# Performance work log

Measured on AMD Instinct MI355X. Metric: run time of the kernel, lower is better.

## Reference

```python
import jax, jax.numpy as jnp
import numpy as np
import math

S, W, H = 256, 128, 768   # sentence, word, hidden (hidden fixed to 768 by PositionalEncoding)
TOPK = 3                  # len(inputs) > 2 branch: fuse 3 nearest sentences


def positional_encoding(length, d_model):
    # Standard sinusoidal PE, identical to the torch buffer construction.
    pos = jnp.arange(length, dtype=jnp.float32)[:, None]                      # [L,1]
    div = jnp.exp(jnp.arange(0, d_model, 2, dtype=jnp.float32)
                  * (-math.log(10000.0) / d_model))                           # [H/2]
    pe = jnp.zeros((length, d_model), dtype=jnp.float32)
    pe = pe.at[:, 0::2].set(jnp.sin(pos * div))
    pe = pe.at[:, 1::2].set(jnp.cos(pos * div))
    return pe


def setup_inputs() -> dict:
    key = jax.random.key(0)
    inputs = jax.random.normal(key, (S, W, H), dtype=jnp.float32)
    return {"inputs": inputs}


def reference(inputs):
    s, w, h = inputs.shape
    # Pairwise L1 distance between the FIRST word vector of each sentence
    # (matmulCell only ever sees x[i,0,:] and k[0,j,:] == inputs[j,0,:]).
    x0 = inputs[:, 0, :]                                                      # [S,H]
    dist = jnp.sum(jnp.abs(x0[:, None, :] - x0[None, :, :]), axis=-1)         # [S,S]
    # torch.sort ascending -> 3 nearest sentences (self included, dist 0)
    idx = jnp.argsort(dist, axis=1)[:, :TOPK]                                 # [S,3] int
    fused = inputs[idx].reshape(s, TOPK * w, h)                               # [S,3W,H]
    # Positional encoding added to both q/v stream and k stream (same tensor;
    # dropout p=0.1 is identity in eval mode).
    x = fused + positional_encoding(TOPK * w, h)[None]                        # [S,3W,H]
    # Scaled dot-product self-attention per row.
    scores = jnp.einsum('slh,smh->slm', x, x) / jnp.sqrt(jnp.float32(h))      # [S,3W,3W]
    attn = jax.nn.softmax(scores, axis=-1)
    out = jnp.einsum('slm,smh->slh', attn, x)                                 # [S,3W,H]
    # D_Attention keeps only the first word-1 rows of each fused output.
    return out[:, :w - 1, :]                                                  # [S,W-1,H]
```

## Files before the change

### kernel.cpp

```cpp
#include <hip/hip_runtime.h>

#define NS 256
#define NW 128
#define NH 768
#define NL 384
#define WH (NW*NH)
#define OUTROWS 127

typedef __attribute__((ext_vector_type(8))) short short8;
typedef __attribute__((ext_vector_type(8))) unsigned short ushort8;
typedef __attribute__((ext_vector_type(4))) float f32x4;

#define XS_STRIDE 72
#define PS_STRIDE 392
#define SMEM_PS   (NL*XS_STRIDE*2)
#define SMEM_RED  (SMEM_PS + 128*PS_STRIDE*2)
#define SMEM_TOTAL (SMEM_RED + 4096)

__device__ __forceinline__ unsigned short bf16b(float f) {
  union { float f; unsigned u; } x; x.f = f;
  return (unsigned short)((x.u + 0x7fffu + ((x.u >> 16) & 1u)) >> 16);
}
__device__ __forceinline__ float b2f(unsigned short h) {
  union { unsigned u; float f; } x; x.u = ((unsigned)h) << 16;
  return x.f;
}

__global__ __launch_bounds__(1024) void k_top3(const float* __restrict__ inp,
                                               int* __restrict__ idxw) {
  const int i = blockIdx.x, t = threadIdx.x;
  __shared__ float xi[772];
  __shared__ float dist[NS];
  __shared__ unsigned long long wkeys[16];
  for (int h = t; h < NH; h += 1024) xi[h + h / 192] = inp[(size_t)i * WH + h];
  __syncthreads();
  const int c = t >> 2, seg = t & 3;
  const float* __restrict__ row = inp + (size_t)c * WH + seg * 192;
  const float* xis = xi + seg * 193;
  float s = 0.f;
  #pragma unroll 4
  for (int h = 0; h < 192; h += 4) {
    float4 v = *(const float4*)(row + h);
    s += fabsf(xis[h]     - v.x) + fabsf(xis[h + 1] - v.y)
       + fabsf(xis[h + 2] - v.z) + fabsf(xis[h + 3] - v.w);
  }
  s += __shfl_xor(s, 1, 64);
  s += __shfl_xor(s, 2, 64);
  if (seg == 0) dist[c] = s;
  __syncthreads();
  for (int k = 0; k < 3; ++k) {
    float d = (t < NS) ? dist[t] : 3.4e38f;
    unsigned long long key = ((unsigned long long)__float_as_uint(d) << 32) | (unsigned)t;
    #pragma unroll
    for (int dd = 1; dd < 64; dd <<= 1) {
      unsigned long long o = __shfl_xor(key, dd, 64);
      key = (o < key) ? o : key;
    }
    if ((t & 63) == 0) wkeys[t >> 6] = key;
    __syncthreads();
    if (t == 0) {
      unsigned long long best = wkeys[0];
      for (int w = 1; w < 16; ++w) if (wkeys[w] < best) best = wkeys[w];
      int bj = (int)(best & 0xffffffffu);
      idxw[i * 3 + k] = bj;
      dist[bj] = 3.4e38f;
    }
    __syncthreads();
  }
}

__global__ __launch_bounds__(256) void k_pe(unsigned short* __restrict__ peb) {
  int gid = blockIdx.x * 256 + threadIdx.x;
  if (gid >= NL * NH) return;
  int l = gid / NH, d = gid - l * NH;
  const float c = -0.011992630687355995f;
  float dv = __expf((float)(d & ~1) * c);
  float ang = (float)l * dv;
  float v = (d & 1) ? cosf(ang) : sinf(ang);
  peb[gid] = bf16b(v);
}

__global__ __launch_bounds__(256) void k_inpb(const float* __restrict__ inp,
                                              unsigned short* __restrict__ inpb) {
  size_t gid = (size_t)blockIdx.x * 256 + threadIdx.x;
  size_t base = gid * 8;
  float4 a = *(const float4*)(inp + base);
  float4 b = *(const float4*)(inp + base + 4);
  ushort8 o;
  o[0] = bf16b(a.x); o[1] = bf16b(a.y); o[2] = bf16b(a.z); o[3] = bf16b(a.w);
  o[4] = bf16b(b.x); o[5] = bf16b(b.y); o[6] = bf16b(b.z); o[7] = bf16b(b.w);
  *(ushort8*)(inpb + base) = o;
}

template<bool BF>
__device__ __forceinline__ void load8(const void* __restrict__ src, size_t off, float* v) {
  if constexpr (BF) {
    ushort8 u = *reinterpret_cast<const ushort8*>((const unsigned short*)src + off);
    #pragma unroll
    for (int j = 0; j < 8; ++j) v[j] = b2f(u[j]);
  } else {
    float4 a = *reinterpret_cast<const float4*>((const float*)src + off);
    float4 b = *reinterpret_cast<const float4*>((const float*)src + off + 4);
    v[0] = a.x; v[1] = a.y; v[2] = a.z; v[3] = a.w;
    v[4] = b.x; v[5] = b.y; v[6] = b.z; v[7] = b.w;
  }
}

template<bool BF>
__global__ __launch_bounds__(512)
void k_attn(const void* __restrict__ xsrc, const unsigned short* __restrict__ peb,
            const int* __restrict__ idxw, float* __restrict__ out) {
  extern __shared__ char smem[];
  unsigned short* Xs = (unsigned short*)smem;
  unsigned short* Ps = (unsigned short*)(smem + SMEM_PS);
  float* red1 = (float*)(smem + SMEM_RED);
  float* red2 = red1 + 512;

  const int s = blockIdx.x;
  const int tid = threadIdx.x;
  const int lane = tid & 63, wid = tid >> 6;
  const int lrow = lane & 15, lhi = lane >> 4;
  const int i0 = idxw[s * 3 + 0], i1 = idxw[s * 3 + 1], i2 = idxw[s * 3 + 2];

  const f32x4 fz = {0.f, 0.f, 0.f, 0.f};
  f32x4 acc[4][6];
  #pragma unroll
  for (int qs = 0; qs < 4; ++qs)
    #pragma unroll
    for (int kf = 0; kf < 6; ++kf) acc[qs][kf] = fz;

  const int qh = wid & 1, kq = wid >> 1;

  for (int hc = 0; hc < 12; ++hc) {
    const int h0 = hc * 64;
    #pragma unroll
    for (int it = 0; it < 6; ++it) {
      const int src = (it < 2) ? i0 : (it < 4 ? i1 : i2);
      const int rl = (tid >> 3) + (it & 1) * 64;
      const int r  = rl + (it >> 1) * 128;
      const int c8 = (tid & 7) * 8;
      float xv[8], pv[8];
      load8<BF>(xsrc, (size_t)src * WH + (size_t)rl * NH + h0 + c8, xv);
      load8<true>(peb, (size_t)r * NH + h0 + c8, pv);
      ushort8 o;
      #pragma unroll
      for (int j = 0; j < 8; ++j) o[j] = bf16b(xv[j] + pv[j]);
      *reinterpret_cast<ushort8*>(&Xs[r * XS_STRIDE + c8]) = o;
    }
    __syncthreads();
    #pragma unroll
    for (int ks = 0; ks < 64; ks += 32) {
      short8 a[4];
      #pragma unroll
      for (int qs = 0; qs < 4; ++qs)
        a[qs] = *reinterpret_cast<const short8*>(&Xs[(qh * 64 + qs * 16 + lrow) * XS_STRIDE + ks + lhi * 8]);
      #pragma unroll
      for (int kf = 0; kf < 6; ++kf) {
        short8 b = *reinterpret_cast<const short8*>(&Xs[(kq * 96 + kf * 16 + lrow) * XS_STRIDE + ks + lhi * 8]);
        #pragma unroll
        for (int qs = 0; qs < 4; ++qs)
          acc[qs][kf] = __builtin_amdgcn_mfma_f32_16x16x32_bf16(a[qs], b, acc[qs][kf], 0, 0, 0);
      }
    }
    __syncthreads();
  }

  const float scale = 0.03608439182435161f;
  float mx[4][4];
  #pragma unroll
  for (int qs = 0; qs < 4; ++qs)
    #pragma unroll
    for (int r = 0; r < 4; ++r) {
      float m = acc[qs][0][r];
      #pragma unroll
      for (int kf = 1; kf < 6; ++kf) m = fmaxf(m, acc[qs][kf][r]);
      #pragma unroll
      for (int d = 1; d < 16; d <<= 1) m = fmaxf(m, __shfl_xor(m, d, 64));
      mx[qs][r] = m;
    }
  if (lrow == 0) {
    #pragma unroll
    for (int qs = 0; qs < 4; ++qs)
      #pragma unroll
      for (int r = 0; r < 4; ++r)
        red1[(qh * 64 + qs * 16 + lhi * 4 + r) * 4 + kq] = mx[qs][r];
  }
  __syncthreads();
  float sm[4][4];
  #pragma unroll
  for (int qs = 0; qs < 4; ++qs)
    #pragma unroll
    for (int r = 0; r < 4; ++r) {
      const int row = qh * 64 + qs * 16 + lhi * 4 + r;
      mx[qs][r] = fmaxf(fmaxf(red1[row * 4 + 0], red1[row * 4 + 1]),
                        fmaxf(red1[row * 4 + 2], red1[row * 4 + 3]));
      sm[qs][r] = 0.f;
    }
  #pragma unroll
  for (int qs = 0; qs < 4; ++qs)
    #pragma unroll
    for (int kf = 0; kf < 6; ++kf)
      #pragma unroll
      for (int r = 0; r < 4; ++r) {
        float p = __expf((acc[qs][kf][r] - mx[qs][r]) * scale);
        acc[qs][kf][r] = p;
        sm[qs][r] += p;
      }
  #pragma unroll
  for (int qs = 0; qs < 4; ++qs)
    #pragma unroll
    for (int r = 0; r < 4; ++r) {
      #pragma unroll
      for (int d = 1; d < 16; d <<= 1) sm[qs][r] += __shfl_xor(sm[qs][r], d, 64);
    }
  if (lrow == 0) {
    #pragma unroll
    for (int qs = 0; qs < 4; ++qs)
      #pragma unroll
      for (int r = 0; r < 4; ++r)
        red2[(qh * 64 + qs * 16 + lhi * 4 + r) * 4 + kq] = sm[qs][r];
  }
  __syncthreads();
  #pragma unroll
  for (int qs = 0; qs < 4; ++qs)
    #pragma unroll
    for (int r = 0; r < 4; ++r) {
      const int row = qh * 64 + qs * 16 + lhi * 4 + r;
      float t = red2[row * 4 + 0] + red2[row * 4 + 1] + red2[row * 4 + 2] + red2[row * 4 + 3];
      sm[qs][r] = 1.0f / t;
    }
  #pragma unroll
  for (int qs = 0; qs < 4; ++qs)
    #pragma unroll
    for (int kf = 0; kf < 6; ++kf)
      #pragma unroll
      for (int r = 0; r < 4; ++r)
        Ps[(qh * 64 + qs * 16 + lhi * 4 + r) * PS_STRIDE + kq * 96 + kf * 16 + lrow] =
            bf16b(acc[qs][kf][r] * sm[qs][r]);
  __syncthreads();

  const int qb = wid & 3, hh = wid >> 2;
  short8 pa[2][12];
  #pragma unroll
  for (int qs = 0; qs < 2; ++qs)
    #pragma unroll
    for (int m0 = 0; m0 < 12; ++m0)
      pa[qs][m0] = *reinterpret_cast<const short8*>(&Ps[(qb * 32 + qs * 16 + lrow) * PS_STRIDE + m0 * 32 + lhi * 8]);

  unsigned short* VT = Xs;
  for (int t4 = 0; t4 < 12; ++t4) {
    const int h0 = t4 * 64;
    #pragma unroll
    for (int it = 0; it < 6; ++it) {
      const int src = (it < 2) ? i0 : (it < 4 ? i1 : i2);
      const int ml = (tid >> 3) + (it & 1) * 64;
      const int m  = ml + (it >> 1) * 128;
      const int c8 = (tid & 7) * 8;
      float xv[8], pv[8];
      load8<BF>(xsrc, (size_t)src * WH + (size_t)ml * NH + h0 + c8, xv);
      load8<true>(peb, (size_t)m * NH + h0 + c8, pv);
      #pragma unroll
      for (int j = 0; j < 8; ++j) {
        const int vr = c8 + j;
        VT[((vr * PS_STRIDE) + m) ^ (((vr >> 3) & 7) << 3)] = bf16b(xv[j] + pv[j]);
      }
    }
    __syncthreads();
    f32x4 o00 = fz, o01 = fz, o10 = fz, o11 = fz;
    #pragma unroll
    for (int m0 = 0; m0 < 12; ++m0) {
      const int vr0 = hh * 32 + lrow, vr1 = vr0 + 16;
      short8 b0 = *reinterpret_cast<const short8*>(
          &VT[((vr0 * PS_STRIDE) + m0 * 32 + lhi * 8) ^ (((vr0 >> 3) & 7) << 3)]);
      short8 b1 = *reinterpret_cast<const short8*>(
          &VT[((vr1 * PS_STRIDE) + m0 * 32 + lhi * 8) ^ (((vr1 >> 3) & 7) << 3)]);
      o00 = __builtin_amdgcn_mfma_f32_16x16x32_bf16(pa[0][m0], b0, o00, 0, 0, 0);
      o01 = __builtin_amdgcn_mfma_f32_16x16x32_bf16(pa[0][m0], b1, o01, 0, 0, 0);
      o10 = __builtin_amdgcn_mfma_f32_16x16x32_bf16(pa[1][m0], b0, o10, 0, 0, 0);
      o11 = __builtin_amdgcn_mfma_f32_16x16x32_bf16(pa[1][m0], b1, o11, 0, 0, 0);
    }
    #pragma unroll
    for (int qs = 0; qs < 2; ++qs)
      #pragma unroll
      for (int hf = 0; hf < 2; ++hf) {
        f32x4 o = (qs == 0) ? (hf == 0 ? o00 : o01) : (hf == 0 ? o10 : o11);
        #pragma unroll
        for (int r = 0; r < 4; ++r) {
          const int q = qb * 32 + qs * 16 + lhi * 4 + r;
          if (q < OUTROWS)
            out[(size_t)s * (OUTROWS * NH) + (size_t)q * NH + h0 + hh * 32 + hf * 16 + lrow] = o[r];
        }
      }
    __syncthreads();
  }
}

extern "C" void kernel_launch(void* const* d_in, const int* in_sizes, int n_in,
                              void* d_out, int out_size, void* d_ws, size_t ws_size,
                              hipStream_t stream) {
  (void)in_sizes; (void)n_in; (void)out_size;
  const float* inp = (const float*)d_in[0];
  float* out = (float*)d_out;
  char* ws = (char*)d_ws;

  unsigned short* peb = (unsigned short*)ws;
  int* idxw           = (int*)(ws + 589824);
  unsigned short* inpb= (unsigned short*)(ws + 592896);
  const bool primary = ws_size >= (size_t)50924544;

  hipLaunchKernelGGL(k_top3, dim3(256), dim3(1024), 0, stream, inp, idxw);
  hipLaunchKernelGGL(k_pe, dim3(1152), dim3(256), 0, stream, peb);

  if (primary) {
    hipLaunchKernelGGL(k_inpb, dim3(12288), dim3(256), 0, stream, inp, inpb);
    hipFuncSetAttribute((const void*)k_attn<true>,
                        hipFuncAttributeMaxDynamicSharedMemorySize, SMEM_TOTAL);
    hipLaunchKernelGGL(k_attn<true>, dim3(256), dim3(512), SMEM_TOTAL, stream,
                       (const void*)inpb, peb, idxw, out);
  } else {
    hipFuncSetAttribute((const void*)k_attn<false>,
                        hipFuncAttributeMaxDynamicSharedMemorySize, SMEM_TOTAL);
    hipLaunchKernelGGL(k_attn<false>, dim3(256), dim3(512), SMEM_TOTAL, stream,
                       (const void*)inp, peb, idxw, out);
  }
}
```

Measured before the change: 138.9 us.

## Use hardware bf16 conversion, swizzle P tile, add MFMA priority hints

Replaces the manual round-to-nearest-even bf16 conversion with the compiler's native __bf16 cast, which can map to a hardware conversion instruction on MI355X. Adds an XOR swizzle to the probability tile in shared memory to reduce bank conflicts on the transposed reads. Raises wave priority around the MFMA loops, vectorizes the softmax reduction reads into float4 loads, and hoists the output address computation. Native conversion may round NaN and edge cases slightly differently, and the priority hints may have little effect.

Result: faster. 136.1 us (-2.0%).

```diff
diff --git a/kernel.cpp b/kernel.cpp
--- a/kernel.cpp
+++ b/kernel.cpp
@@ -9,6 +9,7 @@
 
 typedef __attribute__((ext_vector_type(8))) short short8;
 typedef __attribute__((ext_vector_type(8))) unsigned short ushort8;
+typedef __attribute__((ext_vector_type(8))) __bf16 bf16x8;
 typedef __attribute__((ext_vector_type(4))) float f32x4;
 
 #define XS_STRIDE 72
@@ -24,6 +25,10 @@
 __device__ __forceinline__ float b2f(unsigned short h) {
   union { unsigned u; float f; } x; x.u = ((unsigned)h) << 16;
   return x.f;
+}
+__device__ __forceinline__ unsigned short bfc(float f) {
+  __bf16 h = (__bf16)f;
+  return __builtin_bit_cast(unsigned short, h);
 }
 
 __global__ __launch_bounds__(1024) void k_top3(const float* __restrict__ inp,
@@ -87,8 +92,8 @@
   float4 a = *(const float4*)(inp + base);
   float4 b = *(const float4*)(inp + base + 4);
   ushort8 o;
-  o[0] = bf16b(a.x); o[1] = bf16b(a.y); o[2] = bf16b(a.z); o[3] = bf16b(a.w);
-  o[4] = bf16b(b.x); o[5] = bf16b(b.y); o[6] = bf16b(b.z); o[7] = bf16b(b.w);
+  o[0] = bfc(a.x); o[1] = bfc(a.y); o[2] = bfc(a.z); o[3] = bfc(a.w);
+  o[4] = bfc(b.x); o[5] = bfc(b.y); o[6] = bfc(b.z); o[7] = bfc(b.w);
   *(ushort8*)(inpb + base) = o;
 }
 
@@ -142,12 +147,13 @@
       float xv[8], pv[8];
       load8<BF>(xsrc, (size_t)src * WH + (size_t)rl * NH + h0 + c8, xv);
       load8<true>(peb, (size_t)r * NH + h0 + c8, pv);
-      ushort8 o;
-      #pragma unroll
-      for (int j = 0; j < 8; ++j) o[j] = bf16b(xv[j] + pv[j]);
-      *reinterpret_cast<ushort8*>(&Xs[r * XS_STRIDE + c8]) = o;
-    }
-    __syncthreads();
+      bf16x8 o;
+      #pragma unroll
+      for (int j = 0; j < 8; ++j) o[j] = (__bf16)(xv[j] + pv[j]);
+      *reinterpret_cast<bf16x8*>(&Xs[r * XS_STRIDE + c8]) = o;
+    }
+    __syncthreads();
+    __builtin_amdgcn_s_setprio(1);
     #pragma unroll
     for (int ks = 0; ks < 64; ks += 32) {
       short8 a[4];
@@ -162,6 +168,7 @@
           acc[qs][kf] = __builtin_amdgcn_mfma_f32_16x16x32_bf16(a[qs], b, acc[qs][kf], 0, 0, 0);
       }
     }
+    __builtin_amdgcn_s_setprio(0);
     __syncthreads();
   }
 
@@ -192,8 +199,8 @@
     #pragma unroll
     for (int r = 0; r < 4; ++r) {
       const int row = qh * 64 + qs * 16 + lhi * 4 + r;
-      mx[qs][r] = fmaxf(fmaxf(red1[row * 4 + 0], red1[row * 4 + 1]),
-                        fmaxf(red1[row * 4 + 2], red1[row * 4 + 3]));
+      float4 m0 = *(const float4*)&red1[row * 4];
+      mx[qs][r] = fmaxf(fmaxf(m0.x, m0.y), fmaxf(m0.z, m0.w));
       sm[qs][r] = 0.f;
     }
   #pragma unroll
@@ -226,17 +233,20 @@
     #pragma unroll
     for (int r = 0; r < 4; ++r) {
       const int row = qh * 64 + qs * 16 + lhi * 4 + r;
-      float t = red2[row * 4 + 0] + red2[row * 4 + 1] + red2[row * 4 + 2] + red2[row * 4 + 3];
-      sm[qs][r] = 1.0f / t;
+      float4 s0 = *(const float4*)&red2[row * 4];
+      sm[qs][r] = 1.0f / ((s0.x + s0.y) + (s0.z + s0.w));
     }
   #pragma unroll
   for (int qs = 0; qs < 4; ++qs)
     #pragma unroll
     for (int kf = 0; kf < 6; ++kf)
       #pragma unroll
-      for (int r = 0; r < 4; ++r)
-        Ps[(qh * 64 + qs * 16 + lhi * 4 + r) * PS_STRIDE + kq * 96 + kf * 16 + lrow] =
-            bf16b(acc[qs][kf][r] * sm[qs][r]);
+      for (int r = 0; r < 4; ++r) {
+        const int row = qh * 64 + qs * 16 + lhi * 4 + r;
+        const int col = kq * 96 + kf * 16 + lrow;
+        *(unsigned short*)((char*)Ps + (((row * PS_STRIDE + col) * 2) ^ (((row >> 3) & 7) << 4))) =
+            bfc(acc[qs][kf][r] * sm[qs][r]);
+      }
   __syncthreads();
 
   const int qb = wid & 3, hh = wid >> 2;
@@ -244,8 +254,11 @@
   #pragma unroll
   for (int qs = 0; qs < 2; ++qs)
     #pragma unroll
-    for (int m0 = 0; m0 < 12; ++m0)
-      pa[qs][m0] = *reinterpret_cast<const short8*>(&Ps[(qb * 32 + qs * 16 + lrow) * PS_STRIDE + m0 * 32 + lhi * 8]);
+    for (int m0 = 0; m0 < 12; ++m0) {
+      const int row = qb * 32 + qs * 16 + lrow;
+      pa[qs][m0] = *reinterpret_cast<const short8*>(
+          (const char*)Ps + (((row * PS_STRIDE + m0 * 32 + lhi * 8) * 2) ^ (((row >> 3) & 7) << 4)));
+    }
 
   unsigned short* VT = Xs;
   for (int t4 = 0; t4 < 12; ++t4) {
@@ -262,23 +275,26 @@
       #pragma unroll
       for (int j = 0; j < 8; ++j) {
         const int vr = c8 + j;
-        VT[((vr * PS_STRIDE) + m) ^ (((vr >> 3) & 7) << 3)] = bf16b(xv[j] + pv[j]);
-      }
-    }
-    __syncthreads();
+        VT[((vr * PS_STRIDE) + m) ^ (((vr >> 3) & 7) << 3)] = bfc(xv[j] + pv[j]);
+      }
+    }
+    __syncthreads();
+    __builtin_amdgcn_s_setprio(1);
     f32x4 o00 = fz, o01 = fz, o10 = fz, o11 = fz;
-    #pragma unroll
-    for (int m0 = 0; m0 < 12; ++m0) {
-      const int vr0 = hh * 32 + lrow, vr1 = vr0 + 16;
-      short8 b0 = *reinterpret_cast<const short8*>(
-          &VT[((vr0 * PS_STRIDE) + m0 * 32 + lhi * 8) ^ (((vr0 >> 3) & 7) << 3)]);
-      short8 b1 = *reinterpret_cast<const short8*>(
-          &VT[((vr1 * PS_STRIDE) + m0 * 32 + lhi * 8) ^ (((vr1 >> 3) & 7) << 3)]);
-      o00 = __builtin_amdgcn_mfma_f32_16x16x32_bf16(pa[0][m0], b0, o00, 0, 0, 0);
-      o01 = __builtin_amdgcn_mfma_f32_16x16x32_bf16(pa[0][m0], b1, o01, 0, 0, 0);
-      o10 = __builtin_amdgcn_mfma_f32_16x16x32_bf16(pa[1][m0], b0, o10, 0, 0, 0);
-      o11 = __builtin_amdgcn_mfma_f32_16x16x32_bf16(pa[1][m0], b1, o11, 0, 0, 0);
-    }
+    const int vr0 = hh * 32 + lrow, vr1 = vr0 + 16;
+    const int sw0 = ((vr0 >> 3) & 7) << 4, sw1 = ((vr1 >> 3) & 7) << 4;
+    #pragma unroll
+    for (int mm = 0; mm < 12; ++mm) {
+      const int moff = (mm * 32 + lhi * 8) * 2;
+      short8 b0 = *reinterpret_cast<const short8*>((const char*)VT + ((vr0 * PS_STRIDE * 2 + moff) ^ sw0));
+      short8 b1 = *reinterpret_cast<const short8*>((const char*)VT + ((vr1 * PS_STRIDE * 2 + moff) ^ sw1));
+      o00 = __builtin_amdgcn_mfma_f32_16x16x32_bf16(pa[0][mm], b0, o00, 0, 0, 0);
+      o01 = __builtin_amdgcn_mfma_f32_16x16x32_bf16(pa[0][mm], b1, o01, 0, 0, 0);
+      o10 = __builtin_amdgcn_mfma_f32_16x16x32_bf16(pa[1][mm], b0, o10, 0, 0, 0);
+      o11 = __builtin_amdgcn_mfma_f32_16x16x32_bf16(pa[1][mm], b1, o11, 0, 0, 0);
+    }
+    __builtin_amdgcn_s_setprio(0);
+    float* ob = out + (size_t)s * (OUTROWS * NH) + h0 + hh * 32 + lrow;
     #pragma unroll
     for (int qs = 0; qs < 2; ++qs)
       #pragma unroll
@@ -287,8 +303,7 @@
         #pragma unroll
         for (int r = 0; r < 4; ++r) {
           const int q = qb * 32 + qs * 16 + lhi * 4 + r;
-          if (q < OUTROWS)
-            out[(size_t)s * (OUTROWS * NH) + (size_t)q * NH + h0 + hh * 32 + hf * 16 + lrow] = o[r];
+          if (q < OUTROWS) ob[(size_t)q * NH + hf * 16] = o[r];
         }
       }
     __syncthreads();
```
